# Optimization experiments

Measured on AMD Instinct MI355X. Metric: run time of the kernel, lower is better.

## Reference

```python
import jax, jax.numpy as jnp
import numpy as np

G, P, DEG = 1024, 75, 8            # graphs, nodes per graph, out-degree
N, E = G * P, G * P * DEG
KS, DIM = 5, 2
K = KS ** DIM                      # 25 spline weight matrices
VOX = 4                            # 2x2 voxel grid per graph (size=14 over [0,27.99])


def setup_inputs():
    key = jax.random.key(0)
    ks = jax.random.split(key, 14)
    x = jax.random.uniform(ks[0], (N, 1), dtype=jnp.float32)            # pixel intensities
    src = jnp.repeat(jnp.arange(N, dtype=jnp.int32), DEG)
    dst = (src // P) * P + jax.random.randint(ks[1], (E,), 0, P, dtype=jnp.int32)
    edge_index = jnp.stack([src, dst])                                   # [2,E], within-graph edges
    edge_attr = jax.random.uniform(ks[2], (E, DIM), dtype=jnp.float32)  # Cartesian pseudo-coords in [0,1]
    batch = jnp.repeat(jnp.arange(G, dtype=jnp.int32), P)
    pos = jax.random.uniform(ks[3], (N, DIM), dtype=jnp.float32) * 27.99

    def nrm(k, shape, fan_in):
        return jax.random.normal(k, shape, jnp.float32) / np.float32(np.sqrt(fan_in))

    W1 = nrm(ks[4], (K, 1, 32), 1.0)
    root1 = nrm(ks[5], (1, 32), 1.0)
    b1 = jnp.zeros((32,), jnp.float32)
    W2 = nrm(ks[6], (K, 32, 64), 32.0)
    root2 = nrm(ks[7], (32, 64), 32.0)
    b2 = jnp.zeros((64,), jnp.float32)
    W3 = nrm(ks[8], (K, 64, 64), 64.0)
    root3 = nrm(ks[9], (64, 64), 64.0)
    b3 = jnp.zeros((64,), jnp.float32)
    fc1_w = nrm(ks[10], (4 * 64, 128), 256.0)
    fc1_b = jnp.zeros((128,), jnp.float32)
    fc2_w = nrm(ks[11], (128, 10), 128.0)
    fc2_b = jnp.zeros((10,), jnp.float32)
    return dict(x=x, edge_index=edge_index, edge_attr=edge_attr, batch=batch, pos=pos,
                W1=W1, root1=root1, b1=b1, W2=W2, root2=root2, b2=b2,
                W3=W3, root3=root3, b3=b3,
                fc1_w=fc1_w, fc1_b=fc1_b, fc2_w=fc2_w, fc2_b=fc2_b)


def spline_basis(u):
    """Degree-1 open B-spline basis, dim=2, kernel_size=5. u:[E,2] in [0,1].
    Returns basis [E,4] and flat weight indices [E,4]."""
    p = u * (KS - 1)
    lo = jnp.clip(jnp.floor(p), 0.0, KS - 1)
    frac = p - lo
    lo_i = lo.astype(jnp.int32)
    hi_i = jnp.minimum(lo_i + 1, KS - 1)
    w0 = jnp.stack([1.0 - frac[:, 0], frac[:, 0]], 1)   # [E,2]
    w1 = jnp.stack([1.0 - frac[:, 1], frac[:, 1]], 1)
    i0 = jnp.stack([lo_i[:, 0], hi_i[:, 0]], 1)
    i1 = jnp.stack([lo_i[:, 1], hi_i[:, 1]], 1)
    basis = (w0[:, :, None] * w1[:, None, :]).reshape(-1, 4)      # [E,4]
    idx = (i0[:, :, None] + KS * i1[:, None, :]).reshape(-1, 4)   # [E,4]
    return basis, idx


def spline_conv(h, src, dst, basis, idx, W, root, bias):
    # per-node transform under all K kernel weights: [N,K,O]
    y = jnp.einsum('ni,kio->nko', h, W)
    O = W.shape[2]
    msg = jnp.zeros((src.shape[0], O), h.dtype)
    for s in range(4):  # 4 B-spline corner contributions (fixed small loop)
        msg = msg + basis[:, s:s + 1] * y[src, idx[:, s]]
    agg = jax.ops.segment_sum(msg, dst, num_segments=N)
    deg = jax.ops.segment_sum(jnp.ones((src.shape[0],), h.dtype), dst, num_segments=N)
    agg = agg / jnp.maximum(deg, 1.0)[:, None]          # aggr='mean'
    return agg + h @ root + bias


def reference(x, edge_index, edge_attr, batch, pos,
              W1, root1, b1, W2, root2, b2, W3, root3, b3,
              fc1_w, fc1_b, fc2_w, fc2_b):
    src, dst = edge_index[0], edge_index[1]
    basis, idx = spline_basis(edge_attr)
    h = jax.nn.elu(spline_conv(x, src, dst, basis, idx, W1, root1, b1))
    h = jax.nn.elu(spline_conv(h, src, dst, basis, idx, W2, root2, b2))
    h = jax.nn.elu(spline_conv(h, src, dst, basis, idx, W3, root3, b3))
    # voxel_grid(size=14, start=0, end=27.99) -> 2x2 grid per graph
    vox = jnp.clip((pos / 14.0).astype(jnp.int32), 0, 1)          # [N,2]
    cluster = batch * VOX + vox[:, 0] + 2 * vox[:, 1]
    pooled = jax.ops.segment_max(h, cluster, num_segments=G * VOX)
    pooled = jnp.where(jnp.isneginf(pooled), 0.0, pooled)         # empty voxels -> 0
    graph_x = pooled.reshape(G, VOX * 64)                          # [G, 256]
    graph_x = jax.nn.elu(graph_x @ fc1_w + fc1_b)                  # dropout: eval mode (identity)
    logits = graph_x @ fc2_w + fc2_b
    return jax.nn.log_softmax(logits, axis=1)
```

## Files before the change

### kernel.cpp

```cpp
#include <hip/hip_runtime.h>
#include <math.h>

#define NG 1024
#define NP 75
#define NE_G 600
#define E_TOT 614400
#define NK 25
#define NSEG 1875
#define SST 104
#define YTST 104
#define HST 72

typedef _Float16 half8 __attribute__((ext_vector_type(8)));
typedef float floatx4 __attribute__((ext_vector_type(4)));

#define WS_WT2 0
#define WS_WT3 51200
#define WS_R2T 153600
#define WS_R3T 155648

__device__ __forceinline__ float elu_f(float x) {
    return x > 0.f ? x : (expf(x) - 1.f);
}
__device__ __forceinline__ float h16f(unsigned short b) {
    union { unsigned short u; _Float16 h; } c; c.u = b; return (float)c.h;
}
__device__ __forceinline__ _Float16 bits16(unsigned short b) {
    union { unsigned short u; _Float16 h; } c; c.u = b; return c.h;
}
__device__ __forceinline__ unsigned short f16bits(float v) {
    union { _Float16 h; unsigned short u; } c; c.h = (_Float16)v; return c.u;
}

__global__ void __launch_bounds__(256) prep_weights(
    const float* __restrict__ W2, const float* __restrict__ root2,
    const float* __restrict__ W3, const float* __restrict__ root3,
    _Float16* __restrict__ ws)
{
    int i = blockIdx.x * 256 + threadIdx.x;
    int stride = gridDim.x * 256;
    for (int t = i; t < 25 * 64 * 32; t += stride) {
        int k = t >> 11, o = (t >> 5) & 63, ci = t & 31;
        ws[WS_WT2 + t] = (_Float16)W2[(k * 32 + ci) * 64 + o];
    }
    for (int t = i; t < 25 * 64 * 64; t += stride) {
        int k = t >> 12, o = (t >> 6) & 63, ci = t & 63;
        ws[WS_WT3 + t] = (_Float16)W3[(k * 64 + ci) * 64 + o];
    }
    for (int t = i; t < 64 * 32; t += stride) {
        int o = t >> 5, ci = t & 31;
        ws[WS_R2T + t] = (_Float16)root2[ci * 64 + o];
    }
    for (int t = i; t < 64 * 64; t += stride) {
        int o = t >> 6, ci = t & 63;
        ws[WS_R3T + t] = (_Float16)root3[ci * 64 + o];
    }
}

struct EdgeB { int dl; int kk[4]; unsigned short bas[4]; };
__device__ __forceinline__ EdgeB edge_basis(const float* __restrict__ attr,
                                            const int* __restrict__ eidx,
                                            int g, int e) {
    EdgeB r;
    int ge = g * NE_G + e;
    r.dl = eidx[E_TOT + ge] - g * NP;
    float p0 = attr[2 * ge + 0] * 4.f, p1 = attr[2 * ge + 1] * 4.f;
    float fl0 = fminf(fmaxf(floorf(p0), 0.f), 4.f);
    float fl1 = fminf(fmaxf(floorf(p1), 0.f), 4.f);
    float fr0 = p0 - fl0, fr1 = p1 - fl1;
    int i00 = (int)fl0, i10 = (int)fl1;
    int i01 = min(i00 + 1, 4), i11 = min(i10 + 1, 4);
    float w0a[2] = {1.f - fr0, fr0};
    float w1a[2] = {1.f - fr1, fr1};
    int i0a[2] = {i00, i01};
    int i1a[2] = {i10, i11};
    #pragma unroll
    for (int a = 0; a < 2; ++a)
        #pragma unroll
        for (int b = 0; b < 2; ++b) {
            int s = a * 2 + b;
            r.kk[s] = i0a[a] + 5 * i1a[b];
            r.bas[s] = f16bits(w0a[a] * w1a[b]);
        }
    return r;
}

template<int CIN>
__device__ __forceinline__ void conv_layer(
    const _Float16* __restrict__ Wt,
    const _Float16* __restrict__ rootT,
    const float* __restrict__ bias,
    _Float16* __restrict__ sb_S,
    _Float16* __restrict__ sb_yT,
    _Float16* __restrict__ sb_h,
    const unsigned* __restrict__ sb_list,
    const int* __restrict__ sb_koff,
    const float* __restrict__ sb_rdeg,
    int tid, int lane, int wid)
{
    const int m = lane & 15, q = (lane >> 4) & 3;
    const int o = wid * 16 + m;
    constexpr int KK = CIN / 32;

    half8 Ah[5][KK];
    #pragma unroll
    for (int mt = 0; mt < 5; ++mt)
        #pragma unroll
        for (int kk = 0; kk < KK; ++kk)
            Ah[mt][kk] = *(const half8*)&sb_h[(mt * 16 + m) * HST + kk * 32 + q * 8];
    __syncthreads();

    floatx4 agg[5];
    #pragma unroll
    for (int mt = 0; mt < 5; ++mt) agg[mt] = (floatx4){0.f, 0.f, 0.f, 0.f};

    half8 Bc[KK], Bn[KK];
    #pragma unroll
    for (int kk = 0; kk < KK; ++kk)
        Bc[kk] = *(const half8*)&Wt[(0 * 64 + o) * CIN + kk * 32 + q * 8];

    for (int k = 0; k < NK; ++k) {
        const int jb = sb_koff[k] + tid, kend = sb_koff[k + 1];
        unsigned upre = (jb < kend) ? sb_list[jb] : 0u;
        const _Float16* nb = (k < NK - 1) ? &Wt[((k + 1) * 64 + o) * CIN]
                                          : &rootT[o * CIN];
        #pragma unroll
        for (int kk = 0; kk < KK; ++kk)
            Bn[kk] = *(const half8*)&nb[kk * 32 + q * 8];
        if (k == 0) {
            for (int t = tid; t < 80 * SST / 8; t += 256)
                ((floatx4*)sb_S)[t] = (floatx4){0.f, 0.f, 0.f, 0.f};
        } else {
            for (int j = sb_koff[k - 1] + tid; j < sb_koff[k]; j += 256) {
                unsigned u = sb_list[j];
                sb_S[((u >> 7) & 127) * SST + (u & 127)] = (_Float16)0.f;
            }
        }
        #pragma unroll
        for (int mt = 0; mt < 5; ++mt) {
            floatx4 c = {0.f, 0.f, 0.f, 0.f};
            #pragma unroll
            for (int kk = 0; kk < KK; ++kk)
                c = __builtin_amdgcn_mfma_f32_16x16x32_f16(Ah[mt][kk], Bc[kk], c, 0, 0, 0);
            union { _Float16 h[4]; unsigned long long u64; } p;
            p.h[0] = (_Float16)c[0]; p.h[1] = (_Float16)c[1];
            p.h[2] = (_Float16)c[2]; p.h[3] = (_Float16)c[3];
            *(unsigned long long*)&sb_yT[o * YTST + mt * 16 + q * 4] = p.u64;
        }
        __syncthreads();
        {
            bool first = true;
            for (int j = jb; j < kend; j += 256) {
                unsigned u = first ? upre : sb_list[j];
                first = false;
                if (u >> 16)
                    sb_S[((u >> 7) & 127) * SST + (u & 127)] = bits16((unsigned short)(u >> 16));
            }
        }
        __syncthreads();
        {
            half8 B0 = *(const half8*)&sb_yT[o * YTST + 0 + q * 8];
            half8 B1 = *(const half8*)&sb_yT[o * YTST + 32 + q * 8];
            half8 B2 = *(const half8*)&sb_yT[o * YTST + 64 + q * 8];
            #pragma unroll
            for (int mt = 0; mt < 5; ++mt) {
                half8 a0 = *(const half8*)&sb_S[(mt * 16 + m) * SST + 0 + q * 8];
                half8 a1 = *(const half8*)&sb_S[(mt * 16 + m) * SST + 32 + q * 8];
                half8 a2 = *(const half8*)&sb_S[(mt * 16 + m) * SST + 64 + q * 8];
                floatx4 c = agg[mt];
                c = __builtin_amdgcn_mfma_f32_16x16x32_f16(a0, B0, c, 0, 0, 0);
                c = __builtin_amdgcn_mfma_f32_16x16x32_f16(a1, B1, c, 0, 0, 0);
                c = __builtin_amdgcn_mfma_f32_16x16x32_f16(a2, B2, c, 0, 0, 0);
                agg[mt] = c;
            }
        }
        #pragma unroll
        for (int kk = 0; kk < KK; ++kk) Bc[kk] = Bn[kk];
        __syncthreads();
    }

    float bo = bias[o];
    #pragma unroll
    for (int mt = 0; mt < 5; ++mt) {
        floatx4 c = {0.f, 0.f, 0.f, 0.f};
        #pragma unroll
        for (int kk = 0; kk < KK; ++kk)
            c = __builtin_amdgcn_mfma_f32_16x16x32_f16(Ah[mt][kk], Bc[kk], c, 0, 0, 0);
        #pragma unroll
        for (int r = 0; r < 4; ++r) {
            int n = mt * 16 + q * 4 + r;
            if (n < NP) {
                float v = agg[mt][r] * sb_rdeg[n] + c[r] + bo;
                sb_h[n * HST + o] = (_Float16)elu_f(v);
            }
        }
    }
    for (int p = tid; p < 5 * HST / 2; p += 256)
        ((unsigned*)&sb_h[NP * HST])[p] = 0u;
    __syncthreads();
}

__global__ void __launch_bounds__(256, 4) mnist_spline_fused(
    const float* __restrict__ xg,
    const int* __restrict__ eidx,
    const float* __restrict__ attr,
    const float* __restrict__ pos,
    const float* __restrict__ W1, const float* __restrict__ root1, const float* __restrict__ b1,
    const float* __restrict__ b2, const float* __restrict__ b3,
    const float* __restrict__ fc1w, const float* __restrict__ fc1b,
    const float* __restrict__ fc2w, const float* __restrict__ fc2b,
    const _Float16* __restrict__ ws,
    float* __restrict__ out)
{
    const int g = blockIdx.x;
    const int tid = threadIdx.x;
    const int lane = tid & 63;
    const int wid = tid >> 6;

    __shared__ __align__(16) unsigned char sb_SU[80 * SST * 2];
    __shared__ __align__(16) _Float16 sb_yT[64 * YTST];
    __shared__ __align__(16) unsigned sb_list[NE_G * 4];
    __shared__ int sb_koff[26];
    __shared__ float sb_x[80];
    __shared__ float sb_rdeg[80];
    __shared__ int sb_deg[80];
    __shared__ unsigned sb_vmask[12];
    __shared__ unsigned sb_wsum[8];

    _Float16* sb_S = (_Float16*)sb_SU;
    _Float16* sb_h = (_Float16*)sb_SU;
    unsigned* cnt32 = (unsigned*)sb_SU;
    unsigned short* segoff = (unsigned short*)(sb_SU + 11520);
    _Float16* T1 = (_Float16*)sb_SU;
    _Float16* W1T = (_Float16*)sb_yT;
    float* fc_gx = (float*)(sb_SU + 11776);
    float* fc_part = (float*)(sb_SU + 12800);
    float* fc_z1 = (float*)(sb_SU + 14848);

    for (int p = tid; p < 80; p += 256) sb_deg[p] = 0;
    for (int p = tid; p < NSEG; p += 256) cnt32[p] = 0u;
    for (int p = tid; p < 5 * HST / 2; p += 256)
        ((unsigned*)&sb_h[NP * HST])[p] = 0u;
    for (int p = tid; p < 64 * 12; p += 256) {
        int ch = p / 12, c = p % 12;
        ((unsigned*)sb_yT)[ch * (YTST / 2) + 40 + c] = 0u;
    }
    if (tid < 12) sb_vmask[tid] = 0u;
    __syncthreads();
    for (int p = tid; p < 32 * 32; p += 256) {
        int k = p >> 5, o = p & 31;
        W1T[o * 32 + k] = (k < NK) ? (_Float16)W1[k * 32 + o] : (_Float16)0.f;
    }

    const bool has2 = (tid + 512 < NE_G);
    const int e2i = has2 ? (tid + 512) : tid;
    EdgeB eb0 = edge_basis(attr, eidx, g, tid);
    EdgeB eb1 = edge_basis(attr, eidx, g, tid + 256);
    EdgeB eb2 = edge_basis(attr, eidx, g, e2i);
    atomicAdd(&sb_deg[eb0.dl], 1);
    atomicAdd(&sb_deg[eb1.dl], 1);
    if (has2) atomicAdd(&sb_deg[eb2.dl], 1);
    #pragma unroll
    for (int s = 0; s < 4; ++s) {
        atomicAdd(&cnt32[eb0.kk[s] * NP + eb0.dl], 1u);
        atomicAdd(&cnt32[eb1.kk[s] * NP + eb1.dl], 1u);
        if (has2) atomicAdd(&cnt32[eb2.kk[s] * NP + eb2.dl], 1u);
    }
    for (int n = tid; n < NP; n += 256) {
        int gn = g * NP + n;
        sb_x[n] = xg[gn];
        int v0 = min(max((int)(pos[2 * gn] * (1.f / 14.f)), 0), 1);
        int v1 = min(max((int)(pos[2 * gn + 1] * (1.f / 14.f)), 0), 1);
        int v = v0 + 2 * v1;
        atomicOr(&sb_vmask[v * 3 + (n >> 5)], 1u << (n & 31));
    }
    __syncthreads();

    {
        int base = tid * 8;
        unsigned c8[8], lsum = 0;
        #pragma unroll
        for (int i = 0; i < 8; ++i) {
            int idx = base + i;
            c8[i] = (idx < NSEG) ? cnt32[idx] : 0u;
            lsum += c8[i];
        }
        unsigned v = lsum;
        #pragma unroll
        for (int d = 1; d < 64; d <<= 1) {
            unsigned ov = __shfl_up(v, d);
            if (lane >= d) v += ov;
        }
        if (lane == 63) sb_wsum[wid] = v;
        __syncthreads();
        unsigned wpre = 0;
        for (int w2 = 0; w2 < wid; ++w2) wpre += sb_wsum[w2];
        unsigned run = wpre + v - lsum;
        #pragma unroll
        for (int i = 0; i < 8; ++i) {
            int idx = base + i;
            if (idx < NSEG + 1) segoff[idx] = (unsigned short)run;
            if (idx < NSEG) cnt32[idx] = run;
            run += c8[i];
        }
        if (tid < 80) sb_rdeg[tid] = (tid < NP) ? 1.f / fmaxf((float)sb_deg[tid], 1.f) : 0.f;
    }
    __syncthreads();

    {
        int s0a = tid >> 3;
        int s1a = (tid + 256) >> 3;
        int s2a = e2i >> 3;
        #pragma unroll
        for (int s = 0; s < 4; ++s) {
            unsigned p0 = atomicAdd(&cnt32[eb0.kk[s] * NP + eb0.dl], 1u);
            sb_list[p0] = ((unsigned)eb0.bas[s] << 16) | ((unsigned)eb0.dl << 7) | (unsigned)s0a;
            unsigned p1 = atomicAdd(&cnt32[eb1.kk[s] * NP + eb1.dl], 1u);
            sb_list[p1] = ((unsigned)eb1.bas[s] << 16) | ((unsigned)eb1.dl << 7) | (unsigned)s1a;
            if (has2) {
                unsigned p2 = atomicAdd(&cnt32[eb2.kk[s] * NP + eb2.dl], 1u);
                sb_list[p2] = ((unsigned)eb2.bas[s] << 16) | ((unsigned)eb2.dl << 7) | (unsigned)s2a;
            }
        }
    }
    if (tid < 26) sb_koff[tid] = segoff[min(tid * NP, NSEG)];
    __syncthreads();

    for (int s = tid; s < NSEG; s += 256) {
        int s0 = segoff[s], s1 = segoff[s + 1];
        float tsum = 0.f;
        for (int j = s0; j < s1; ++j) {
            unsigned u = sb_list[j];
            if (!(u >> 16)) continue;
            int src = u & 127;
            float bsum = h16f((unsigned short)(u >> 16));
            for (int j2 = j + 1; j2 < s1; ++j2) {
                unsigned u2 = sb_list[j2];
                if ((u2 & 127) == (unsigned)src && (u2 >> 16)) {
                    bsum += h16f((unsigned short)(u2 >> 16));
                    sb_list[j2] = u2 & 0xFFFFu;
                }
            }
            sb_list[j] = ((unsigned)f16bits(bsum) << 16) | (u & 0xFFFFu);
            tsum += bsum * sb_x[src];
        }
        int k = s / NP, d = s - k * NP;
        T1[d * 40 + k] = (_Float16)tsum;
    }
    for (int t = tid; t < NP * 15 + 5 * 40; t += 256) {
        int d, k;
        if (t < NP * 15) { d = t / 15; k = NK + t % 15; }
        else { int t2 = t - NP * 15; d = NP + t2 / 40; k = t2 % 40; }
        T1[d * 40 + k] = (_Float16)0.f;
    }
    __syncthreads();

    {
        floatx4 l1c[5];
        const int m = lane & 15, q = (lane >> 4) & 3;
        const int o = wid * 16 + m;
        if (wid < 2) {
            half8 Bw = *(const half8*)&W1T[o * 32 + q * 8];
            #pragma unroll
            for (int mt = 0; mt < 5; ++mt) {
                half8 a = *(const half8*)&T1[(mt * 16 + m) * 40 + q * 8];
                floatx4 c = {0.f, 0.f, 0.f, 0.f};
                l1c[mt] = __builtin_amdgcn_mfma_f32_16x16x32_f16(a, Bw, c, 0, 0, 0);
            }
        }
        __syncthreads();
        if (wid < 2) {
            float rt = root1[o], bo = b1[o];
            #pragma unroll
            for (int mt = 0; mt < 5; ++mt)
                #pragma unroll
                for (int r = 0; r < 4; ++r) {
                    int n = mt * 16 + q * 4 + r;
                    if (n < NP) {
                        float v = l1c[mt][r] * sb_rdeg[n] + sb_x[n] * rt + bo;
                        sb_h[n * HST + o] = (_Float16)elu_f(v);
                    }
                }
        }
    }
    __syncthreads();

    conv_layer<32>(ws + WS_WT2, ws + WS_R2T, b2, sb_S, sb_yT, sb_h,
                   sb_list, sb_koff, sb_rdeg, tid, lane, wid);
    conv_layer<64>(ws + WS_WT3, ws + WS_R3T, b3, sb_S, sb_yT, sb_h,
                   sb_list, sb_koff, sb_rdeg, tid, lane, wid);

    {
        int v = wid, o = lane;
        float mval = -INFINITY;
        #pragma unroll 25
        for (int n = 0; n < NP; ++n) {
            float val = (float)sb_h[n * HST + o];
            bool sel = (sb_vmask[v * 3 + (n >> 5)] >> (n & 31)) & 1;
            mval = sel ? fmaxf(mval, val) : mval;
        }
        fc_gx[v * 64 + o] = (mval == -INFINITY) ? 0.f : mval;
    }
    __syncthreads();

    {
        float acc0 = 0.f, acc1 = 0.f;
        #pragma unroll 8
        for (int i = 0; i < 64; ++i) {
            int ii = wid * 64 + i;
            float xv = fc_gx[ii];
            acc0 += xv * fc1w[ii * 128 + lane];
            acc1 += xv * fc1w[ii * 128 + 64 + lane];
        }
        fc_part[wid * 128 + lane] = acc0;
        fc_part[wid * 128 + 64 + lane] = acc1;
    }
    __syncthreads();
    if (tid < 128) {
        float v = fc_part[tid] + fc_part[128 + tid] + fc_part[256 + tid] + fc_part[384 + tid]
                + fc1b[tid];
        fc_z1[tid] = elu_f(v);
    }
    __syncthreads();

    if (wid == 0) {
        int o = lane & 15, sg = lane >> 4;
        float acc = 0.f;
        if (o < 10) {
            #pragma unroll 8
            for (int i = sg * 32; i < sg * 32 + 32; ++i)
                acc += fc_z1[i] * fc2w[i * 10 + o];
        }
        acc += __shfl_xor(acc, 16);
        acc += __shfl_xor(acc, 32);
        float logit = (o < 10) ? (acc + fc2b[o]) : 0.f;
        float lv = (o < 10) ? logit : -INFINITY;
        float mx = lv;
        #pragma unroll
        for (int d = 1; d < 16; d <<= 1) mx = fmaxf(mx, __shfl_xor(mx, d));
        float ex = (o < 10) ? expf(logit - mx) : 0.f;
        float se = ex;
        #pragma unroll
        for (int d = 1; d < 16; d <<= 1) se += __shfl_xor(se, d);
        if (lane < 10) out[g * 10 + lane] = logit - mx - logf(se);
    }
}

extern "C" void kernel_launch(void* const* d_in, const int* in_sizes, int n_in,
                              void* d_out, int out_size, void* d_ws, size_t ws_size,
                              hipStream_t stream) {
    const float* xg    = (const float*)d_in[0];
    const int*   eidx  = (const int*)d_in[1];
    const float* attr  = (const float*)d_in[2];
    const float* pos   = (const float*)d_in[4];
    const float* W1    = (const float*)d_in[5];
    const float* root1 = (const float*)d_in[6];
    const float* b1    = (const float*)d_in[7];
    const float* W2    = (const float*)d_in[8];
    const float* root2 = (const float*)d_in[9];
    const float* b2    = (const float*)d_in[10];
    const float* W3    = (const float*)d_in[11];
    const float* root3 = (const float*)d_in[12];
    const float* b3    = (const float*)d_in[13];
    const float* fc1w  = (const float*)d_in[14];
    const float* fc1b  = (const float*)d_in[15];
    const float* fc2w  = (const float*)d_in[16];
    const float* fc2b  = (const float*)d_in[17];
    float* out = (float*)d_out;
    _Float16* ws = (_Float16*)d_ws;

    prep_weights<<<160, 256, 0, stream>>>(W2, root2, W3, root3, ws);
    mnist_spline_fused<<<NG, 256, 0, stream>>>(
        xg, eidx, attr, pos, W1, root1, b1, b2, b3,
        fc1w, fc1b, fc2w, fc2b, ws, out);
}
```

Before: 219.9 us.

## Drop weight prep kernel, load fp32 weights directly and shrink LDS strides

```diff
diff --git a/kernel.cpp b/kernel.cpp
--- a/kernel.cpp
+++ b/kernel.cpp
@@ -7,18 +7,13 @@
 #define E_TOT 614400
 #define NK 25
 #define NSEG 1875
-#define SST 104
-#define YTST 104
+#define SST 80
+#define YTST 80
 #define HST 72
 
 typedef _Float16 half8 __attribute__((ext_vector_type(8)));
 typedef float floatx4 __attribute__((ext_vector_type(4)));
 
-#define WS_WT2 0
-#define WS_WT3 51200
-#define WS_R2T 153600
-#define WS_R3T 155648
-
 __device__ __forceinline__ float elu_f(float x) {
     return x > 0.f ? x : (expf(x) - 1.f);
 }
@@ -31,30 +26,13 @@
 __device__ __forceinline__ unsigned short f16bits(float v) {
     union { _Float16 h; unsigned short u; } c; c.h = (_Float16)v; return c.u;
 }
-
-__global__ void __launch_bounds__(256) prep_weights(
-    const float* __restrict__ W2, const float* __restrict__ root2,
-    const float* __restrict__ W3, const float* __restrict__ root3,
-    _Float16* __restrict__ ws)
-{
-    int i = blockIdx.x * 256 + threadIdx.x;
-    int stride = gridDim.x * 256;
-    for (int t = i; t < 25 * 64 * 32; t += stride) {
-        int k = t >> 11, o = (t >> 5) & 63, ci = t & 31;
-        ws[WS_WT2 + t] = (_Float16)W2[(k * 32 + ci) * 64 + o];
-    }
-    for (int t = i; t < 25 * 64 * 64; t += stride) {
-        int k = t >> 12, o = (t >> 6) & 63, ci = t & 63;
-        ws[WS_WT3 + t] = (_Float16)W3[(k * 64 + ci) * 64 + o];
-    }
-    for (int t = i; t < 64 * 32; t += stride) {
-        int o = t >> 5, ci = t & 31;
-        ws[WS_R2T + t] = (_Float16)root2[ci * 64 + o];
-    }
-    for (int t = i; t < 64 * 64; t += stride) {
-        int o = t >> 6, ci = t & 63;
-        ws[WS_R3T + t] = (_Float16)root3[ci * 64 + o];
-    }
+__device__ __forceinline__ half8 ldB(const float* __restrict__ p) {
+    half8 b;
+    b[0] = (_Float16)p[0];   b[1] = (_Float16)p[64];
+    b[2] = (_Float16)p[128]; b[3] = (_Float16)p[192];
+    b[4] = (_Float16)p[256]; b[5] = (_Float16)p[320];
+    b[6] = (_Float16)p[384]; b[7] = (_Float16)p[448];
+    return b;
 }
 
 struct EdgeB { int dl; int kk[4]; unsigned short bas[4]; };
@@ -87,8 +65,7 @@
 
 template<int CIN>
 __device__ __forceinline__ void conv_layer(
-    const _Float16* __restrict__ Wt,
-    const _Float16* __restrict__ rootT,
+    const float* __restrict__ Wf, const float* __restrict__ rootf,
     const float* __restrict__ bias,
     _Float16* __restrict__ sb_S,
     _Float16* __restrict__ sb_yT,
@@ -101,6 +78,7 @@
     const int m = lane & 15, q = (lane >> 4) & 3;
     const int o = wid * 16 + m;
     constexpr int KK = CIN / 32;
+    const half8 zero8 = {};
 
     half8 Ah[5][KK];
     #pragma unroll
@@ -117,16 +95,18 @@
     half8 Bc[KK], Bn[KK];
     #pragma unroll
     for (int kk = 0; kk < KK; ++kk)
-        Bc[kk] = *(const half8*)&Wt[(0 * 64 + o) * CIN + kk * 32 + q * 8];
+        Bc[kk] = ldB(Wf + (0 * CIN + kk * 32 + q * 8) * 64 + o);
 
     for (int k = 0; k < NK; ++k) {
         const int jb = sb_koff[k] + tid, kend = sb_koff[k + 1];
         unsigned upre = (jb < kend) ? sb_list[jb] : 0u;
-        const _Float16* nb = (k < NK - 1) ? &Wt[((k + 1) * 64 + o) * CIN]
-                                          : &rootT[o * CIN];
-        #pragma unroll
-        for (int kk = 0; kk < KK; ++kk)
-            Bn[kk] = *(const half8*)&nb[kk * 32 + q * 8];
+        #pragma unroll
+        for (int kk = 0; kk < KK; ++kk) {
+            const float* p = (k < NK - 1)
+                ? (Wf + ((k + 1) * CIN + kk * 32 + q * 8) * 64 + o)
+                : (rootf + (kk * 32 + q * 8) * 64 + o);
+            Bn[kk] = ldB(p);
+        }
         if (k == 0) {
             for (int t = tid; t < 80 * SST / 8; t += 256)
                 ((floatx4*)sb_S)[t] = (floatx4){0.f, 0.f, 0.f, 0.f};
@@ -161,12 +141,14 @@
         {
             half8 B0 = *(const half8*)&sb_yT[o * YTST + 0 + q * 8];
             half8 B1 = *(const half8*)&sb_yT[o * YTST + 32 + q * 8];
-            half8 B2 = *(const half8*)&sb_yT[o * YTST + 64 + q * 8];
+            half8 B2 = zero8;
+            if (q < 2) B2 = *(const half8*)&sb_yT[o * YTST + 64 + q * 8];
             #pragma unroll
             for (int mt = 0; mt < 5; ++mt) {
                 half8 a0 = *(const half8*)&sb_S[(mt * 16 + m) * SST + 0 + q * 8];
                 half8 a1 = *(const half8*)&sb_S[(mt * 16 + m) * SST + 32 + q * 8];
-                half8 a2 = *(const half8*)&sb_S[(mt * 16 + m) * SST + 64 + q * 8];
+                half8 a2 = zero8;
+                if (q < 2) a2 = *(const half8*)&sb_S[(mt * 16 + m) * SST + 64 + q * 8];
                 floatx4 c = agg[mt];
                 c = __builtin_amdgcn_mfma_f32_16x16x32_f16(a0, B0, c, 0, 0, 0);
                 c = __builtin_amdgcn_mfma_f32_16x16x32_f16(a1, B1, c, 0, 0, 0);
@@ -206,10 +188,10 @@
     const float* __restrict__ attr,
     const float* __restrict__ pos,
     const float* __restrict__ W1, const float* __restrict__ root1, const float* __restrict__ b1,
-    const float* __restrict__ b2, const float* __restrict__ b3,
+    const float* __restrict__ W2, const float* __restrict__ root2, const float* __restrict__ b2,
+    const float* __restrict__ W3, const float* __restrict__ root3, const float* __restrict__ b3,
     const float* __restrict__ fc1w, const float* __restrict__ fc1b,
     const float* __restrict__ fc2w, const float* __restrict__ fc2b,
-    const _Float16* __restrict__ ws,
     float* __restrict__ out)
 {
     const int g = blockIdx.x;
@@ -218,39 +200,36 @@
     const int wid = tid >> 6;
 
     __shared__ __align__(16) unsigned char sb_SU[80 * SST * 2];
-    __shared__ __align__(16) _Float16 sb_yT[64 * YTST];
+    __shared__ __align__(16) unsigned char sb_yU[64 * YTST * 2];
     __shared__ __align__(16) unsigned sb_list[NE_G * 4];
     __shared__ int sb_koff[26];
-    __shared__ float sb_x[80];
     __shared__ float sb_rdeg[80];
-    __shared__ int sb_deg[80];
     __shared__ unsigned sb_vmask[12];
     __shared__ unsigned sb_wsum[8];
 
     _Float16* sb_S = (_Float16*)sb_SU;
     _Float16* sb_h = (_Float16*)sb_SU;
+    _Float16* sb_yT = (_Float16*)sb_yU;
     unsigned* cnt32 = (unsigned*)sb_SU;
-    unsigned short* segoff = (unsigned short*)(sb_SU + 11520);
     _Float16* T1 = (_Float16*)sb_SU;
-    _Float16* W1T = (_Float16*)sb_yT;
     float* fc_gx = (float*)(sb_SU + 11776);
-    float* fc_part = (float*)(sb_SU + 12800);
-    float* fc_z1 = (float*)(sb_SU + 14848);
+    _Float16* W1T = (_Float16*)sb_yU;
+    unsigned short* segoff = (unsigned short*)(sb_yU + 2048);
+    float* sb_x = (float*)(sb_yU + 5824);
+    int* sb_deg = (int*)(sb_yU + 6144);
+    float* fc_part = (float*)sb_yU;
+    float* fc_z1 = (float*)(sb_yU + 2048);
 
     for (int p = tid; p < 80; p += 256) sb_deg[p] = 0;
     for (int p = tid; p < NSEG; p += 256) cnt32[p] = 0u;
     for (int p = tid; p < 5 * HST / 2; p += 256)
         ((unsigned*)&sb_h[NP * HST])[p] = 0u;
-    for (int p = tid; p < 64 * 12; p += 256) {
-        int ch = p / 12, c = p % 12;
-        ((unsigned*)sb_yT)[ch * (YTST / 2) + 40 + c] = 0u;
-    }
     if (tid < 12) sb_vmask[tid] = 0u;
-    __syncthreads();
     for (int p = tid; p < 32 * 32; p += 256) {
         int k = p >> 5, o = p & 31;
         W1T[o * 32 + k] = (k < NK) ? (_Float16)W1[k * 32 + o] : (_Float16)0.f;
     }
+    __syncthreads();
 
     const bool has2 = (tid + 512 < NE_G);
     const int e2i = has2 ? (tid + 512) : tid;
@@ -385,9 +364,9 @@
     }
     __syncthreads();
 
-    conv_layer<32>(ws + WS_WT2, ws + WS_R2T, b2, sb_S, sb_yT, sb_h,
+    conv_layer<32>(W2, root2, b2, sb_S, sb_yT, sb_h,
                    sb_list, sb_koff, sb_rdeg, tid, lane, wid);
-    conv_layer<64>(ws + WS_WT3, ws + WS_R3T, b3, sb_S, sb_yT, sb_h,
+    conv_layer<64>(W3, root3, b3, sb_S, sb_yT, sb_h,
                    sb_list, sb_koff, sb_rdeg, tid, lane, wid);
 
     {
@@ -467,10 +446,8 @@
     const float* fc2w  = (const float*)d_in[16];
     const float* fc2b  = (const float*)d_in[17];
     float* out = (float*)d_out;
-    _Float16* ws = (_Float16*)d_ws;
-
-    prep_weights<<<160, 256, 0, stream>>>(W2, root2, W3, root3, ws);
+
     mnist_spline_fused<<<NG, 256, 0, stream>>>(
-        xg, eidx, attr, pos, W1, root1, b1, b2, b3,
-        fc1w, fc1b, fc2w, fc2b, ws, out);
-}
+        xg, eidx, attr, pos, W1, root1, b1, W2, root2, b2, W3, root3, b3,
+        fc1w, fc1b, fc2w, fc2b, out);
+}
```

New measurement: 216.7 us. Within noise of the previous version (-1.5%).
